# Optimization experiments

Measured on AMD Instinct MI355X. Metric: run time of the kernel, lower is better.

Reference implementation:

```python
import jax, jax.numpy as jnp
import numpy as np
from jax import lax

HID = 96              # hidden_dim (C)
DM  = 2 * HID         # SS2D d_model (real+imag interleaved channels)
DI  = 2 * DM          # d_inner (expand=2, VMamba default)
N   = 16              # d_state
K   = 4               # scan directions
R   = (DM + 15) // 16 # dt_rank = ceil(d_model/16)
B_, H_, W_ = 1, 64, 64


def _layernorm(x, w, b, eps=1e-5):
    m = x.mean(-1, keepdims=True)
    v = ((x - m) ** 2).mean(-1, keepdims=True)
    return (x - m) * lax.rsqrt(v + eps) * w + b


def _selective_scan(xs, delta, A, Bs, Cs):
    # xs, delta: (B,K,D,L); A: (K,D,N); Bs, Cs: (B,K,N,L)
    def step(h, inp):
        dt, Bt, Ct, ut = inp                              # (B,K,D),(B,K,N),(B,K,N),(B,K,D)
        dA = jnp.exp(dt[..., None] * A[None])             # (B,K,D,N)
        h = h * dA + dt[..., None] * Bt[:, :, None, :] * ut[..., None]
        y = jnp.einsum('bkdn,bkn->bkd', h, Ct)
        return h, y
    inputs = (jnp.moveaxis(delta, -1, 0), jnp.moveaxis(Bs, -1, 0),
              jnp.moveaxis(Cs, -1, 0), jnp.moveaxis(xs, -1, 0))
    h0 = jnp.zeros(xs.shape[:3] + (N,), xs.dtype)
    _, ys = lax.scan(step, h0, inputs)                    # (L,B,K,D)
    return jnp.moveaxis(ys, 0, -1)                        # (B,K,D,L)


def _forward_core(x, x_proj_w, dt_w, dt_b, A_logs, Ds):
    # x: (B, DI, H, W) -- 4-direction cross-scan (VMamba SS2D)
    B, D, H, W = x.shape
    L = H * W
    x_hw = x.reshape(B, D, L)
    x_wh = x.transpose(0, 1, 3, 2).reshape(B, D, L)
    x_hwwh = jnp.stack([x_hw, x_wh], axis=1)                    # (B,2,D,L)
    xs = jnp.concatenate([x_hwwh, jnp.flip(x_hwwh, -1)], 1)     # (B,4,D,L)
    x_dbl = jnp.einsum('bkdl,kcd->bkcl', xs, x_proj_w)          # (B,K,R+2N,L)
    dts, Bs, Cs = jnp.split(x_dbl, [R, R + N], axis=2)
    dts = jnp.einsum('bkrl,kdr->bkdl', dts, dt_w)
    delta = jax.nn.softplus(dts + dt_b[None, :, :, None])
    A = -jnp.exp(A_logs.reshape(K, D, N))
    ys = _selective_scan(xs, delta, A, Bs, Cs)
    out_y = ys + Ds.reshape(K, D)[None, :, :, None] * xs        # (B,4,D,L)
    inv_y = jnp.flip(out_y[:, 2:4], -1)
    tr = lambda t: t.reshape(B, D, W, H).transpose(0, 1, 3, 2).reshape(B, D, L)
    y = out_y[:, 0] + inv_y[:, 0] + tr(out_y[:, 1]) + tr(inv_y[:, 1])
    return y.transpose(0, 2, 1).reshape(B, H, W, D)


def _ss2d(x, in_proj_w, conv_w, conv_b, x_proj_w, dt_w, dt_b,
          A_logs, Ds, out_norm_w, out_norm_b, out_proj_w):
    # x: (B, H, Wf, DM)
    xz = x @ in_proj_w.T                                        # (B,H,Wf,2*DI)
    xc, z = jnp.split(xz, 2, axis=-1)
    xc = xc.transpose(0, 3, 1, 2)                               # (B,DI,H,Wf)
    xc = lax.conv_general_dilated(xc, conv_w, (1, 1), 'SAME',
                                  feature_group_count=DI,
                                  dimension_numbers=('NCHW', 'OIHW', 'NCHW'))
    xc = jax.nn.silu(xc + conv_b[None, :, None, None])
    y = _forward_core(xc, x_proj_w, dt_w, dt_b, A_logs, Ds)     # (B,H,Wf,DI)
    y = _layernorm(y, out_norm_w, out_norm_b)
    y = y * jax.nn.silu(z)
    return y @ out_proj_w.T                                     # (B,H,Wf,DM)


def _freq_vss(x, in_proj_w, conv_w, conv_b, x_proj_w, dt_w, dt_b,
              A_logs, Ds, out_norm_w, out_norm_b, out_proj_w):
    B, H, W, C = x.shape
    xf = jnp.fft.rfft2(x, axes=(1, 2), norm='ortho')            # (B,H,Wf,C) complex
    Wf = xf.shape[2]
    # interleave real/imag into channels: (B,H,Wf,C,2) -> (B,H,Wf,2C)
    x1 = jnp.stack([xf.real, xf.imag], axis=4).reshape(B, H, Wf, 2 * C)
    att = _ss2d(x1, in_proj_w, conv_w, conv_b, x_proj_w, dt_w, dt_b,
                A_logs, Ds, out_norm_w, out_norm_b, out_proj_w)
    att = att.reshape(B, H, Wf, C, 2)
    attc = lax.complex(att[..., 0], att[..., 1])
    x1r = jnp.fft.irfft2(attc, s=(H, W), axes=(1, 2), norm='ortho')
    return x + x1r                                              # residual (drop_path=0)


def setup_inputs() -> dict:
    key = jax.random.key(0)
    ks = jax.random.split(key, 8)
    s = 0.02
    return {
        'x': jax.random.normal(ks[0], (B_, H_, W_, HID), jnp.float32),
        'in_proj_w': jax.random.normal(ks[1], (2 * DI, DM), jnp.float32) * s,
        'conv_w': jax.random.normal(ks[2], (DI, 1, 3, 3), jnp.float32) * s,
        'conv_b': jnp.zeros((DI,), jnp.float32),
        'x_proj_w': jax.random.normal(ks[3], (K, R + 2 * N, DI), jnp.float32) * s,
        'dt_w': jax.random.normal(ks[4], (K, DI, R), jnp.float32) * s,
        'dt_b': jax.random.normal(ks[5], (K, DI), jnp.float32) * 0.1,
        'A_logs': jnp.tile(jnp.log(jnp.arange(1, N + 1, dtype=jnp.float32))[None], (K * DI, 1)),
        'Ds': jnp.ones((K * DI,), jnp.float32),
        'out_norm_w': jnp.ones((DI,), jnp.float32),
        'out_norm_b': jnp.zeros((DI,), jnp.float32),
        'out_proj_w': jax.random.normal(ks[6], (DM, DI), jnp.float32) * s,
    }


def reference(x, in_proj_w, conv_w, conv_b, x_proj_w, dt_w, dt_b,
              A_logs, Ds, out_norm_w, out_norm_b, out_proj_w):
    return _freq_vss(x, in_proj_w, conv_w, conv_b, x_proj_w, dt_w, dt_b,
                     A_logs, Ds, out_norm_w, out_norm_b, out_proj_w)
```

## Files before the change

### kernel.cpp

```cpp
#include <hip/hip_runtime.h>
#include <hip/hip_bf16.h>

#define LQ   2112
#define DQ   384
#define NST  16
#define HQ   64
#define WFQ  33
#define CQ   96
#define SC   66
#define KDN  24576

#define AIPW  0
#define ACW   147456
#define ACB   150912
#define AXPW  151296
#define ADTW  218880
#define ADTB  237312
#define AANEG 238848
#define ADS   263424
#define ANW   264960
#define ANB   265344
#define AOPW  265728
#define ARTOT 339456

#define OFF_FFT   339456
#define OFF_XZ    744960
#define OFF_XCV   2366976
#define OFF_G     3177984
#define OFF_SUMDT 3549696
#define OFF_HEND  3651072
#define OFF_YS    5273088

#define P_ZR  0
#define P_ZI  202752

static __device__ __forceinline__ float u2f(unsigned short u)
{ union { unsigned int i; float f; } v; v.i = ((unsigned int)u) << 16; return v.f; }

static __device__ __forceinline__ float ldin(const void* p, int o, int isbf)
{
    if (isbf) return u2f(((const unsigned short*)p)[o]);
    return ((const float*)p)[o];
}

static __device__ __forceinline__ int isbf_of(const void* ds)
{ return (((const unsigned int*)ds)[0] == 0x3F803F80u) ? 1 : 0; }

__global__ __launch_bounds__(256) void k_convert_all(
    const void* __restrict__ ipw,
    const void* __restrict__ cw,  const void* __restrict__ cb,
    const void* __restrict__ xpw, const void* __restrict__ dtw,
    const void* __restrict__ dtb, const void* __restrict__ alog,
    const void* __restrict__ ds,  const void* __restrict__ nw,
    const void* __restrict__ nb,  const void* __restrict__ opw,
    float* __restrict__ arena)
{
    int isbf = isbf_of(ds);
    int t = blockIdx.x * 256 + threadIdx.x;
    int o = t;
    if (o < 147456) { arena[t] = ldin(ipw, o, isbf); return; }  o -= 147456;
    if (o < 3456)   { arena[t] = ldin(cw, o, isbf);  return; }  o -= 3456;
    if (o < 384)    { arena[t] = ldin(cb, o, isbf);  return; }  o -= 384;
    if (o < 67584)  { arena[t] = ldin(xpw, o, isbf); return; }  o -= 67584;
    if (o < 18432)  { arena[t] = ldin(dtw, o, isbf); return; }  o -= 18432;
    if (o < 1536)   { arena[t] = ldin(dtb, o, isbf); return; }  o -= 1536;
    if (o < 24576)  { arena[t] = -expf(ldin(alog, o, isbf)); return; }  o -= 24576;
    if (o < 1536)   { arena[t] = ldin(ds, o, isbf);  return; }  o -= 1536;
    if (o < 384)    { arena[t] = ldin(nw, o, isbf);  return; }  o -= 384;
    if (o < 384)    { arena[t] = ldin(nb, o, isbf);  return; }  o -= 384;
    arena[t] = ldin(opw, o, isbf);
}

__global__ __launch_bounds__(256) void k_rfftw(const void* __restrict__ x, const void* __restrict__ ds,
                                               float* __restrict__ Zr, float* __restrict__ Zi)
{
    __shared__ float tc[64], ts[64];
    if (threadIdx.x < 64) {
        float ang = -6.283185307179586f * (float)threadIdx.x / 64.f;
        float s, c; __sincosf(ang, &s, &c); tc[threadIdx.x] = c; ts[threadIdx.x] = s;
    }
    __syncthreads();
    const int isbf = isbf_of(ds);
    int tid = blockIdx.x * 256 + threadIdx.x;
    int c = tid % CQ; int f = (tid / CQ) % WFQ; int h = tid / (CQ * WFQ);
    const int base = h * 64 * CQ + c;
    float zr = 0.f, zi = 0.f; int j = 0;
    for (int w = 0; w < 64; w++) {
        float xv = ldin(x, base + w * CQ, isbf);
        zr += xv * tc[j]; zi += xv * ts[j];
        j += f; j &= 63;
    }
    Zr[tid] = zr; Zi[tid] = zi;
}

__global__ __launch_bounds__(256) void k_ffth(const float* __restrict__ Zr, const float* __restrict__ Zi,
                                              float* __restrict__ x1)
{
    __shared__ float tc[64], ts[64];
    if (threadIdx.x < 64) {
        float ang = -6.283185307179586f * (float)threadIdx.x / 64.f;
        float s, c; __sincosf(ang, &s, &c); tc[threadIdx.x] = c; ts[threadIdx.x] = s;
    }
    __syncthreads();
    int tid = blockIdx.x * 256 + threadIdx.x;
    int c = tid % CQ; int f = (tid / CQ) % WFQ; int u = tid / (CQ * WFQ);
    float xr = 0.f, xi = 0.f; int j = 0;
    int base = f * CQ + c;
    for (int h = 0; h < 64; h++) {
        float zr = Zr[base + h * (WFQ * CQ)];
        float zi = Zi[base + h * (WFQ * CQ)];
        xr += zr * tc[j] - zi * ts[j];
        xi += zr * ts[j] + zi * tc[j];
        j += u; j &= 63;
    }
    int l = u * WFQ + f;
    x1[l * 192 + 2 * c]     = xr * (1.f / 64.f);
    x1[l * 192 + 2 * c + 1] = xi * (1.f / 64.f);
}

typedef __attribute__((ext_vector_type(8))) __bf16 bf16x8;
typedef __attribute__((ext_vector_type(4))) float f32x4;

__global__ __launch_bounds__(256) void k_gemm(const float* __restrict__ A, const float* __restrict__ W,
                                              float* __restrict__ C, int N, int K, int sW, int sC)
{
    W += (size_t)blockIdx.z * sW; C += (size_t)blockIdx.z * sC;
    __shared__ __bf16 Asm[64 * 40];
    __shared__ __bf16 Bsm[64 * 40];
    const int tid = threadIdx.x;
    const int bm = blockIdx.y * 64, bn = blockIdx.x * 64;
    const int wv = tid >> 6, lane = tid & 63;
    const int srow = tid >> 2, skk = (tid & 3) * 8;
    const int fm = lane & 15, fq = lane >> 4;
    f32x4 acc0 = {0.f, 0.f, 0.f, 0.f}, acc1 = acc0, acc2 = acc0, acc3 = acc0;
    const __bf16* afp = Asm + (wv * 16 + fm) * 40 + fq * 8;
    const __bf16* bfp = Bsm + fm * 40 + fq * 8;
    for (int k0 = 0; k0 < K; k0 += 32) {
        {
            const float* ap = A + (size_t)(bm + srow) * K + k0 + skk;
            float4 a0 = *(const float4*)ap, a1 = *(const float4*)(ap + 4);
            bf16x8 v = { (__bf16)a0.x, (__bf16)a0.y, (__bf16)a0.z, (__bf16)a0.w,
                         (__bf16)a1.x, (__bf16)a1.y, (__bf16)a1.z, (__bf16)a1.w };
            *(bf16x8*)(Asm + srow * 40 + skk) = v;
        }
        {
            float4 b0 = {0.f,0.f,0.f,0.f}, b1 = b0;
            if (bn + srow < N) {
                const float* wp = W + (size_t)(bn + srow) * K + k0 + skk;
                b0 = *(const float4*)wp; b1 = *(const float4*)(wp + 4);
            }
            bf16x8 v = { (__bf16)b0.x, (__bf16)b0.y, (__bf16)b0.z, (__bf16)b0.w,
                         (__bf16)b1.x, (__bf16)b1.y, (__bf16)b1.z, (__bf16)b1.w };
            *(bf16x8*)(Bsm + srow * 40 + skk) = v;
        }
        __syncthreads();
        bf16x8 af = *(const bf16x8*)afp;
        bf16x8 fb0 = *(const bf16x8*)(bfp);
        bf16x8 fb1 = *(const bf16x8*)(bfp + 16 * 40);
        bf16x8 fb2 = *(const bf16x8*)(bfp + 32 * 40);
        bf16x8 fb3 = *(const bf16x8*)(bfp + 48 * 40);
        acc0 = __builtin_amdgcn_mfma_f32_16x16x32_bf16(af, fb0, acc0, 0, 0, 0);
        acc1 = __builtin_amdgcn_mfma_f32_16x16x32_bf16(af, fb1, acc1, 0, 0, 0);
        acc2 = __builtin_amdgcn_mfma_f32_16x16x32_bf16(af, fb2, acc2, 0, 0, 0);
        acc3 = __builtin_amdgcn_mfma_f32_16x16x32_bf16(af, fb3, acc3, 0, 0, 0);
        __syncthreads();
    }
    const int m0 = bm + wv * 16 + fq * 4;
#pragma unroll
    for (int nt = 0; nt < 4; nt++) {
        f32x4 a = (nt == 0) ? acc0 : ((nt == 1) ? acc1 : ((nt == 2) ? acc2 : acc3));
        int n = bn + nt * 16 + fm;
        if (n < N) {
#pragma unroll
            for (int r = 0; r < 4; r++)
                C[(size_t)(m0 + r) * N + n] = a[r];
        }
    }
}

__global__ __launch_bounds__(256) void k_conv(const float* __restrict__ xz,
                                              const float* __restrict__ ar,
                                              float* __restrict__ xcv)
{
    int tid = blockIdx.x * 256 + threadIdx.x;
    int d = tid % DQ; int l = tid / DQ;
    int h = l / WFQ; int f = l % WFQ;
    float acc = ar[ACB + d];
#pragma unroll
    for (int ky = 0; ky < 3; ky++) {
        int hh = h + ky - 1;
        if (hh < 0 || hh >= HQ) continue;
#pragma unroll
        for (int kx = 0; kx < 3; kx++) {
            int ff = f + kx - 1;
            if (ff < 0 || ff >= WFQ) continue;
            acc += ar[ACW + d * 9 + ky * 3 + kx] * xz[(size_t)(hh * WFQ + ff) * 768 + d];
        }
    }
    float sig = 1.f / (1.f + __expf(-acc));
    xcv[tid] = acc * sig;
}

static __device__ __forceinline__ float softplus_f(float a)
{
    return (a > 15.f) ? a : __logf(1.f + __expf(a));
}

template<int KK> static __device__ __forceinline__ int chunk_l0(int s)
{
    if (KK == 0) return s * 32;
    if (KK == 1) return (s & 1) * 1056 + (s >> 1);
    if (KK == 2) return 2111 - s * 32;
    return 2111 - (s & 1) * 1056 - (s >> 1);
}
template<int KK> static __device__ __forceinline__ int chunk_stp()
{
    if (KK == 0) return 1;
    if (KK == 1) return 33;
    if (KK == 2) return -1;
    return -33;
}

template<int KK, int PASS2> static __device__ __forceinline__ void scan_body(
    const float* __restrict__ xcv, const float* __restrict__ G, const float* __restrict__ ar,
    float* __restrict__ hend, float* __restrict__ sumdt, float* __restrict__ ysum,
    float* __restrict__ dtL, float* __restrict__ duL)
{
    const int s = blockIdx.x, db = blockIdx.y;
    const int lane = threadIdx.x;
    const int d = lane & 15, ng = lane >> 4;
    const int stp = chunk_stp<KK>();
    const int l0 = chunk_l0<KK>(s);
    const float* Gk = G + (size_t)KK * (LQ * 44);

    {
        const int st = lane & 31;
        const int jb = (lane >> 5) * 8;
        const int lt = l0 + stp * st;
        const float* gr = Gk + lt * 44;
        float4 g0 = *(const float4*)(gr);
        float4 g1 = *(const float4*)(gr + 4);
        float4 g2 = *(const float4*)(gr + 8);
        const float* ub = xcv + (size_t)lt * DQ + db * 16 + jb;
        float uu[8];
        *(float4*)(uu)     = *(const float4*)(ub);
        *(float4*)(uu + 4) = *(const float4*)(ub + 4);
#pragma unroll 4
        for (int j = 0; j < 8; j++) {
            const int kdj = KK * DQ + db * 16 + jb + j;
            const float* wp = ar + ADTW + kdj * 12;
            float acc = ar[ADTB + kdj]
                + wp[0] * g0.x + wp[1] * g0.y + wp[2]  * g0.z + wp[3]  * g0.w
                + wp[4] * g1.x + wp[5] * g1.y + wp[6]  * g1.z + wp[7]  * g1.w
                + wp[8] * g2.x + wp[9] * g2.y + wp[10] * g2.z + wp[11] * g2.w;
            float dtv = softplus_f(acc);
            dtL[st * 17 + jb + j] = dtv;
            duL[st * 17 + jb + j] = dtv * uu[j];
        }
    }
    if (!PASS2 && KK == 0 && lane < 32) {
        float4 z4 = make_float4(0.f, 0.f, 0.f, 0.f);
        float* zp = ysum + (size_t)(l0 + lane) * DQ + db * 16;
        *(float4*)zp = z4; *(float4*)(zp + 4) = z4;
        *(float4*)(zp + 8) = z4; *(float4*)(zp + 12) = z4;
    }
    __syncthreads();

    const int kd = KK * DQ + db * 16 + d;
    const int kdn = kd * NST + 4 * ng;
    const float4 Av = *(const float4*)(ar + AANEG + kdn);
    float h0 = 0.f, h1 = 0.f, h2 = 0.f, h3 = 0.f;
    if (PASS2) {
        float4 hh = *(const float4*)(hend + (size_t)s * KDN + kdn);
        h0 = hh.x; h1 = hh.y; h2 = hh.z; h3 = hh.w;
    }

#pragma unroll 4
    for (int i = 0; i < 32; i++) {
        const int l = l0 + stp * i;
        float dt = dtL[i * 17 + d];
        float du = duL[i * 17 + d];
        float4 bv = *(const float4*)(Gk + l * 44 + 12 + 4 * ng);
        h0 = h0 * __expf(dt * Av.x) + du * bv.x;
        h1 = h1 * __expf(dt * Av.y) + du * bv.y;
        h2 = h2 * __expf(dt * Av.z) + du * bv.z;
        h3 = h3 * __expf(dt * Av.w) + du * bv.w;
        if (PASS2) {
            float4 cv = *(const float4*)(Gk + l * 44 + 28 + 4 * ng);
            float yp = h0 * cv.x + h1 * cv.y + h2 * cv.z + h3 * cv.w;
            yp += __shfl_xor(yp, 16);
            yp += __shfl_xor(yp, 32);
            if (ng == 0) atomicAdd(&ysum[(size_t)l * DQ + db * 16 + d], yp);
        }
    }

    if (!PASS2) {
        *(float4*)(hend + (size_t)s * KDN + kdn) = make_float4(h0, h1, h2, h3);
        float sd = 0.f;
#pragma unroll
        for (int t = 0; t < 8; t++) sd += dtL[(ng * 8 + t) * 17 + d];
        sd += __shfl_xor(sd, 16);
        sd += __shfl_xor(sd, 32);
        if (ng == 0) sumdt[s * 1536 + kd] = sd;
    }
}

__global__ __launch_bounds__(64, 8) void k_scan1(const float* __restrict__ xcv, const float* __restrict__ G,
                                                 const float* __restrict__ ar,
                                                 float* __restrict__ hend, float* __restrict__ sumdt,
                                                 float* __restrict__ ysum)
{
    __shared__ float smem[2 * 32 * 17];
    float* dtL = smem; float* duL = smem + 32 * 17;
    switch (blockIdx.z) {
        case 0: scan_body<0, 0>(xcv, G, ar, hend, sumdt, ysum, dtL, duL); break;
        case 1: scan_body<1, 0>(xcv, G, ar, hend, sumdt, ysum, dtL, duL); break;
        case 2: scan_body<2, 0>(xcv, G, ar, hend, sumdt, ysum, dtL, duL); break;
        default: scan_body<3, 0>(xcv, G, ar, hend, sumdt, ysum, dtL, duL); break;
    }
}

__global__ __launch_bounds__(64, 8) void k_scan2(const float* __restrict__ xcv, const float* __restrict__ G,
                                                 const float* __restrict__ ar,
                                                 float* __restrict__ hend, float* __restrict__ sumdt,
                                                 float* __restrict__ ysum)
{
    __shared__ float smem[2 * 32 * 17];
    float* dtL = smem; float* duL = smem + 32 * 17;
    switch (blockIdx.z) {
        case 0: scan_body<0, 1>(xcv, G, ar, hend, sumdt, ysum, dtL, duL); break;
        case 1: scan_body<1, 1>(xcv, G, ar, hend, sumdt, ysum, dtL, duL); break;
        case 2: scan_body<2, 1>(xcv, G, ar, hend, sumdt, ysum, dtL, duL); break;
        default: scan_body<3, 1>(xcv, G, ar, hend, sumdt, ysum, dtL, duL); break;
    }
}

__global__ __launch_bounds__(256) void k_comb(const float* __restrict__ ar, const float* __restrict__ sumdt,
                                              float* __restrict__ hend)
{
    int tid = blockIdx.x * 256 + threadIdx.x;
    int kd = tid >> 4;
    float Av = ar[AANEG + tid];
    float hp = 0.f;
    for (int s = 0; s < SC; s++) {
        float he = hend[(size_t)s * KDN + tid];
        hend[(size_t)s * KDN + tid] = hp;
        hp = hp * __expf(Av * sumdt[s * 1536 + kd]) + he;
    }
}

__global__ __launch_bounds__(128) void k_lnmul(const float* __restrict__ ysum, const float* __restrict__ xcv,
                                               const float* __restrict__ xz, const float* __restrict__ ar,
                                               float* __restrict__ ym)
{
    int l = blockIdx.x; int tid = threadIdx.x;
    float v[3]; float s1 = 0.f, s2 = 0.f;
#pragma unroll
    for (int j = 0; j < 3; j++) {
        int d = tid + j * 128;
        size_t idx = (size_t)l * DQ + d;
        float sd = ar[ADS + d] + ar[ADS + DQ + d] + ar[ADS + 2 * DQ + d] + ar[ADS + 3 * DQ + d];
        float a = ysum[idx] + sd * xcv[idx];
        v[j] = a; s1 += a; s2 += a * a;
    }
#pragma unroll
    for (int off = 1; off < 64; off <<= 1) { s1 += __shfl_xor(s1, off); s2 += __shfl_xor(s2, off); }
    __shared__ float sh[4];
    if ((tid & 63) == 0) { sh[(tid >> 6) * 2] = s1; sh[(tid >> 6) * 2 + 1] = s2; }
    __syncthreads();
    s1 = sh[0] + sh[2]; s2 = sh[1] + sh[3];
    float m = s1 * (1.f / 384.f);
    float var = s2 * (1.f / 384.f) - m * m;
    float rs = rsqrtf(var + 1e-5f);
#pragma unroll
    for (int j = 0; j < 3; j++) {
        int d = tid + j * 128;
        float z = xz[(size_t)l * 768 + 384 + d];
        float sig = 1.f / (1.f + __expf(-z));
        ym[(size_t)l * DQ + d] = ((v[j] - m) * rs * ar[ANW + d] + ar[ANB + d]) * (z * sig);
    }
}

__global__ __launch_bounds__(256) void k_iffth(const float* __restrict__ att,
                                               float* __restrict__ Yr, float* __restrict__ Yi)
{
    __shared__ float tc[64], ts[64];
    if (threadIdx.x < 64) {
        float ang = 6.283185307179586f * (float)threadIdx.x / 64.f;
        float s, c; __sincosf(ang, &s, &c); tc[threadIdx.x] = c; ts[threadIdx.x] = s;
    }
    __syncthreads();
    int tid = blockIdx.x * 256 + threadIdx.x;
    int c = tid % CQ; int f = (tid / CQ) % WFQ; int hp = tid / (CQ * WFQ);
    float yr = 0.f, yi = 0.f; int j = 0;
    for (int h = 0; h < 64; h++) {
        const float* ap = att + (size_t)(h * WFQ + f) * 192 + 2 * c;
        float arv = ap[0], aiv = ap[1];
        yr += arv * tc[j] - aiv * ts[j];
        yi += arv * ts[j] + aiv * tc[j];
        j += hp; j &= 63;
    }
    Yr[tid] = yr * 0.125f;
    Yi[tid] = yi * 0.125f;
}

__global__ __launch_bounds__(256) void k_irfft_res(const float* __restrict__ Yr, const float* __restrict__ Yi,
                                                   const void* __restrict__ x, const void* __restrict__ ds,
                                                   void* __restrict__ out)
{
    __shared__ float tc[64], ts[64];
    if (threadIdx.x < 64) {
        float ang = 6.283185307179586f * (float)threadIdx.x / 64.f;
        float s, c; __sincosf(ang, &s, &c); tc[threadIdx.x] = c; ts[threadIdx.x] = s;
    }
    __syncthreads();
    const int isbf = isbf_of(ds);
    int tid = blockIdx.x * 256 + threadIdx.x;
    int c = tid % CQ; int w = (tid / CQ) % 64; int h = tid / (CQ * 64);
    const float* yr = Yr + h * (WFQ * CQ) + c;
    const float* yi = Yi + h * (WFQ * CQ) + c;
    float acc = yr[0];
    acc += ((w & 1) ? -1.f : 1.f) * yr[32 * CQ];
    float a2 = 0.f; int j = w & 63;
    for (int f = 1; f < 32; f++) {
        a2 += yr[f * CQ] * tc[j] - yi[f * CQ] * ts[j];
        j += w; j &= 63;
    }
    acc += 2.f * a2;
    float val = ldin(x, tid, isbf) + 0.125f * acc;
    if (isbf) ((__hip_bfloat16*)out)[tid] = __float2bfloat16(val);
    else      ((float*)out)[tid] = val;
}

extern "C" void kernel_launch(void* const* d_in, const int* in_sizes, int n_in,
                              void* d_out, int out_size, void* d_ws, size_t ws_size,
                              hipStream_t stream)
{
    float* ws    = (float*)d_ws;
    float* ar    = ws;
    float* Zr    = ws + OFF_FFT + P_ZR;
    float* Zi    = ws + OFF_FFT + P_ZI;
    float* xz    = ws + OFF_XZ;
    float* xcv   = ws + OFF_XCV;
    float* G     = ws + OFF_G;
    float* sumdt = ws + OFF_SUMDT;
    float* hend  = ws + OFF_HEND;
    float* YS    = ws + OFF_YS;

    float* x1   = YS;
    float* ysum = YS;
    float* ym   = hend;
    float* att  = xcv;

    k_convert_all<<<1326, 256, 0, stream>>>(d_in[1], d_in[2], d_in[3], d_in[4], d_in[5],
                                            d_in[6], d_in[7], d_in[8], d_in[9], d_in[10], d_in[11], ar);
    k_rfftw<<<792, 256, 0, stream>>>(d_in[0], d_in[8], Zr, Zi);
    k_ffth<<<792, 256, 0, stream>>>(Zr, Zi, x1);
    k_gemm<<<dim3(12, 33, 1), 256, 0, stream>>>(x1, ar + AIPW, xz, 768, 192, 0, 0);
    k_conv<<<3168, 256, 0, stream>>>(xz, ar, xcv);
    k_gemm<<<dim3(1, 33, 4), 256, 0, stream>>>(xcv, ar + AXPW, G, 44, 384, 44 * 384, LQ * 44);
    k_scan1<<<dim3(SC, 24, 4), 64, 0, stream>>>(xcv, G, ar, hend, sumdt, ysum);
    k_comb<<<96, 256, 0, stream>>>(ar, sumdt, hend);
    k_scan2<<<dim3(SC, 24, 4), 64, 0, stream>>>(xcv, G, ar, hend, sumdt, ysum);
    k_lnmul<<<LQ, 128, 0, stream>>>(ysum, xcv, xz, ar, ym);
    k_gemm<<<dim3(3, 33, 1), 256, 0, stream>>>(ym, ar + AOPW, att, 192, 384, 0, 0);
    k_iffth<<<792, 256, 0, stream>>>(att, Zr, Zi);
    k_irfft_res<<<1536, 256, 0, stream>>>(Zr, Zi, d_in[0], d_in[8], d_out);
}
```

Before: 224.4 us.

## Merge weight conversion with W-axis rfft, batch two positions per conv thread

The weight-conversion kernel and the W-direction rfft kernel are merged into one launch, with the block index choosing which role a block takes, removing one kernel launch and its serialization gap. The depthwise conv now has each thread compute two adjacent positions while holding the nine taps in registers, halving the grid and the weight reloads. The scan inner loop unroll rises from 4 to 8. The merged kernel carries shared-memory setup for every block, and the larger unroll may raise register pressure.

```diff
diff --git a/kernel.cpp b/kernel.cpp
--- a/kernel.cpp
+++ b/kernel.cpp
@@ -46,42 +46,39 @@
 static __device__ __forceinline__ int isbf_of(const void* ds)
 { return (((const unsigned int*)ds)[0] == 0x3F803F80u) ? 1 : 0; }
 
-__global__ __launch_bounds__(256) void k_convert_all(
-    const void* __restrict__ ipw,
+__global__ __launch_bounds__(256) void k_cvt_rfftw(
+    const void* __restrict__ x,   const void* __restrict__ ipw,
     const void* __restrict__ cw,  const void* __restrict__ cb,
     const void* __restrict__ xpw, const void* __restrict__ dtw,
     const void* __restrict__ dtb, const void* __restrict__ alog,
     const void* __restrict__ ds,  const void* __restrict__ nw,
     const void* __restrict__ nb,  const void* __restrict__ opw,
-    float* __restrict__ arena)
-{
-    int isbf = isbf_of(ds);
-    int t = blockIdx.x * 256 + threadIdx.x;
-    int o = t;
-    if (o < 147456) { arena[t] = ldin(ipw, o, isbf); return; }  o -= 147456;
-    if (o < 3456)   { arena[t] = ldin(cw, o, isbf);  return; }  o -= 3456;
-    if (o < 384)    { arena[t] = ldin(cb, o, isbf);  return; }  o -= 384;
-    if (o < 67584)  { arena[t] = ldin(xpw, o, isbf); return; }  o -= 67584;
-    if (o < 18432)  { arena[t] = ldin(dtw, o, isbf); return; }  o -= 18432;
-    if (o < 1536)   { arena[t] = ldin(dtb, o, isbf); return; }  o -= 1536;
-    if (o < 24576)  { arena[t] = -expf(ldin(alog, o, isbf)); return; }  o -= 24576;
-    if (o < 1536)   { arena[t] = ldin(ds, o, isbf);  return; }  o -= 1536;
-    if (o < 384)    { arena[t] = ldin(nw, o, isbf);  return; }  o -= 384;
-    if (o < 384)    { arena[t] = ldin(nb, o, isbf);  return; }  o -= 384;
-    arena[t] = ldin(opw, o, isbf);
-}
-
-__global__ __launch_bounds__(256) void k_rfftw(const void* __restrict__ x, const void* __restrict__ ds,
-                                               float* __restrict__ Zr, float* __restrict__ Zi)
-{
+    float* __restrict__ arena, float* __restrict__ Zr, float* __restrict__ Zi)
+{
+    const int isbf = isbf_of(ds);
+    if (blockIdx.x < 1326) {
+        int t = blockIdx.x * 256 + threadIdx.x;
+        int o = t;
+        if (o < 147456) { arena[t] = ldin(ipw, o, isbf); return; }  o -= 147456;
+        if (o < 3456)   { arena[t] = ldin(cw, o, isbf);  return; }  o -= 3456;
+        if (o < 384)    { arena[t] = ldin(cb, o, isbf);  return; }  o -= 384;
+        if (o < 67584)  { arena[t] = ldin(xpw, o, isbf); return; }  o -= 67584;
+        if (o < 18432)  { arena[t] = ldin(dtw, o, isbf); return; }  o -= 18432;
+        if (o < 1536)   { arena[t] = ldin(dtb, o, isbf); return; }  o -= 1536;
+        if (o < 24576)  { arena[t] = -expf(ldin(alog, o, isbf)); return; }  o -= 24576;
+        if (o < 1536)   { arena[t] = ldin(ds, o, isbf);  return; }  o -= 1536;
+        if (o < 384)    { arena[t] = ldin(nw, o, isbf);  return; }  o -= 384;
+        if (o < 384)    { arena[t] = ldin(nb, o, isbf);  return; }  o -= 384;
+        arena[t] = ldin(opw, o, isbf);
+        return;
+    }
     __shared__ float tc[64], ts[64];
     if (threadIdx.x < 64) {
         float ang = -6.283185307179586f * (float)threadIdx.x / 64.f;
         float s, c; __sincosf(ang, &s, &c); tc[threadIdx.x] = c; ts[threadIdx.x] = s;
     }
     __syncthreads();
-    const int isbf = isbf_of(ds);
-    int tid = blockIdx.x * 256 + threadIdx.x;
+    int tid = (blockIdx.x - 1326) * 256 + threadIdx.x;
     int c = tid % CQ; int f = (tid / CQ) % WFQ; int h = tid / (CQ * WFQ);
     const int base = h * 64 * CQ + c;
     float zr = 0.f, zi = 0.f; int j = 0;
@@ -183,22 +180,31 @@
                                               float* __restrict__ xcv)
 {
     int tid = blockIdx.x * 256 + threadIdx.x;
-    int d = tid % DQ; int l = tid / DQ;
-    int h = l / WFQ; int f = l % WFQ;
-    float acc = ar[ACB + d];
-#pragma unroll
-    for (int ky = 0; ky < 3; ky++) {
-        int hh = h + ky - 1;
-        if (hh < 0 || hh >= HQ) continue;
-#pragma unroll
-        for (int kx = 0; kx < 3; kx++) {
-            int ff = f + kx - 1;
-            if (ff < 0 || ff >= WFQ) continue;
-            acc += ar[ACW + d * 9 + ky * 3 + kx] * xz[(size_t)(hh * WFQ + ff) * 768 + d];
-        }
-    }
-    float sig = 1.f / (1.f + __expf(-acc));
-    xcv[tid] = acc * sig;
+    int d = tid % DQ; int lp = tid / DQ;
+    int l0 = lp * 2;
+    float w9[9];
+#pragma unroll
+    for (int i = 0; i < 9; i++) w9[i] = ar[ACW + d * 9 + i];
+    float cb = ar[ACB + d];
+#pragma unroll
+    for (int q = 0; q < 2; q++) {
+        int l = l0 + q;
+        int h = l / WFQ; int f = l % WFQ;
+        float acc = cb;
+#pragma unroll
+        for (int ky = 0; ky < 3; ky++) {
+            int hh = h + ky - 1;
+            if (hh < 0 || hh >= HQ) continue;
+#pragma unroll
+            for (int kx = 0; kx < 3; kx++) {
+                int ff = f + kx - 1;
+                if (ff < 0 || ff >= WFQ) continue;
+                acc += w9[ky * 3 + kx] * xz[(size_t)(hh * WFQ + ff) * 768 + d];
+            }
+        }
+        float sig = 1.f / (1.f + __expf(-acc));
+        xcv[(size_t)l * DQ + d] = acc * sig;
+    }
 }
 
 static __device__ __forceinline__ float softplus_f(float a)
@@ -275,7 +281,7 @@
         h0 = hh.x; h1 = hh.y; h2 = hh.z; h3 = hh.w;
     }
 
-#pragma unroll 4
+#pragma unroll 8
     for (int i = 0; i < 32; i++) {
         const int l = l0 + stp * i;
         float dt = dtL[i * 17 + d];
@@ -452,12 +458,12 @@
     float* ym   = hend;
     float* att  = xcv;
 
-    k_convert_all<<<1326, 256, 0, stream>>>(d_in[1], d_in[2], d_in[3], d_in[4], d_in[5],
-                                            d_in[6], d_in[7], d_in[8], d_in[9], d_in[10], d_in[11], ar);
-    k_rfftw<<<792, 256, 0, stream>>>(d_in[0], d_in[8], Zr, Zi);
+    k_cvt_rfftw<<<2118, 256, 0, stream>>>(d_in[0], d_in[1], d_in[2], d_in[3], d_in[4], d_in[5],
+                                          d_in[6], d_in[7], d_in[8], d_in[9], d_in[10], d_in[11],
+                                          ar, Zr, Zi);
     k_ffth<<<792, 256, 0, stream>>>(Zr, Zi, x1);
     k_gemm<<<dim3(12, 33, 1), 256, 0, stream>>>(x1, ar + AIPW, xz, 768, 192, 0, 0);
-    k_conv<<<3168, 256, 0, stream>>>(xz, ar, xcv);
+    k_conv<<<1584, 256, 0, stream>>>(xz, ar, xcv);
     k_gemm<<<dim3(1, 33, 4), 256, 0, stream>>>(xcv, ar + AXPW, G, 44, 384, 44 * 384, LQ * 44);
     k_scan1<<<dim3(SC, 24, 4), 64, 0, stream>>>(xcv, G, ar, hend, sumdt, ysum);
     k_comb<<<96, 256, 0, stream>>>(ar, sumdt, hend);
```

New measurement: 223.3 us. No clear change (-0.5%).
